# Optimization experiments

Hardware: AMD Instinct MI355X
Metric: run time of the kernel (lower is better)

Reference implementation:

```python
import jax, jax.numpy as jnp
import numpy as np

NUM_CHARTS = 16
LATENT_DIM = 128
RANK = 128
BATCH = 131072


def _init_weight(key, out_dim, in_dim):
    # nn.init.eye_ on top-left block, then += 0.01 * randn (identity-ish init)
    w = jnp.zeros((out_dim, in_dim), jnp.float32)
    m = min(out_dim, in_dim)
    w = w.at[jnp.arange(m), jnp.arange(m)].set(1.0)
    return w + 0.01 * jax.random.normal(key, (out_dim, in_dim), jnp.float32)


def setup_inputs() -> dict:
    key = jax.random.key(0)
    ks = jax.random.split(key, 3 + 2 * NUM_CHARTS)
    z_n = jax.random.normal(ks[0], (BATCH, LATENT_DIM), jnp.float32)
    source_idx = jax.random.randint(ks[1], (BATCH,), 0, NUM_CHARTS, dtype=jnp.int64 if jax.config.jax_enable_x64 else jnp.int32)
    target_idx = jax.random.randint(ks[2], (BATCH,), 0, NUM_CHARTS, dtype=source_idx.dtype)
    # encoder weights: [C, R, D] (torch Linear weight layout [out, in])
    enc_w = jnp.stack([_init_weight(ks[3 + i], RANK, LATENT_DIM) for i in range(NUM_CHARTS)])
    # decoder weights: [C, D, R]
    dec_w = jnp.stack([_init_weight(ks[3 + NUM_CHARTS + i], LATENT_DIM, RANK) for i in range(NUM_CHARTS)])
    c_param = jnp.zeros((NUM_CHARTS, RANK), jnp.float32)
    d_param = jnp.zeros((NUM_CHARTS, LATENT_DIM), jnp.float32)
    return {"z_n": z_n, "source_idx": source_idx, "target_idx": target_idx,
            "enc_w": enc_w, "dec_w": dec_w, "c_param": c_param, "d_param": d_param}


def _apply_per_chart(x, chart_idx, weights):
    # x: [B, in], weights: [C, out, in] -> [B, out]
    # Loop over the small fixed chart count; each chart does one dense GEMM,
    # results routed by mask-select (same math as gather/compute/scatter).
    C = weights.shape[0]
    out = jnp.zeros((x.shape[0], weights.shape[1]), x.dtype)
    for c in range(C):
        yc = x @ weights[c].T  # [B, out]
        out = jnp.where((chart_idx == c)[:, None], yc, out)
    return out


def reference(z_n, source_idx, target_idx, enc_w, dec_w, c_param, d_param):
    # lift_to_global: per-chart encode + bias c[src]
    h = _apply_per_chart(z_n, source_idx, enc_w) + c_param[source_idx]  # [B, R]
    # project_from_global: per-chart decode + bias d[tgt]
    z_out = _apply_per_chart(h, target_idx, dec_w) + d_param[target_idx]  # [B, D]
    return z_out
```

## Files before the change

### kernel.cpp

```cpp
#include <hip/hip_runtime.h>
#include <hip/hip_bf16.h>

#define NB     131072
#define NCH    16
#define NPAIR  256
#define LDW    136
#define LDH    136
#define LDO    132
#define CAP    1024

#define WS_HIST   0
#define WS_OFF    256
#define WS_SORTED 528
#define WS_BYTES  ((WS_SORTED + NB) * 4)

typedef short short8 __attribute__((ext_vector_type(8)));
typedef float f32x4  __attribute__((ext_vector_type(4)));

__device__ __forceinline__ short bfbits(float x) {
    union { __hip_bfloat16 h; short s; } u;
    u.h = __float2bfloat16(x);
    return u.s;
}

__device__ __forceinline__ short8 cvt_frag(const float* __restrict__ p) {
    const f32x4 lo = *(const f32x4*)p;
    const f32x4 hi = *(const f32x4*)(p + 4);
    short8 r;
    r[0] = bfbits(lo[0]); r[1] = bfbits(lo[1]); r[2] = bfbits(lo[2]); r[3] = bfbits(lo[3]);
    r[4] = bfbits(hi[0]); r[5] = bfbits(hi[1]); r[6] = bfbits(hi[2]); r[7] = bfbits(hi[3]);
    return r;
}

__global__ void k_init(int* __restrict__ hist) {
    hist[threadIdx.x] = 0;
}

__global__ __launch_bounds__(256) void k_hist(const int* __restrict__ si,
                                              const int* __restrict__ ti,
                                              int* __restrict__ hist) {
    __shared__ int sh[NPAIR];
    const int t = threadIdx.x;
    sh[t] = 0;
    __syncthreads();
    const int base = blockIdx.x * 1024 + t;
#pragma unroll
    for (int j = 0; j < 4; ++j) {
        const int i = base + j * 256;
        const int k = (si[i] * NCH + ti[i]) & (NPAIR - 1);
        atomicAdd(&sh[k], 1);
    }
    __syncthreads();
    if (sh[t]) atomicAdd(&hist[t], sh[t]);
}

__global__ __launch_bounds__(256) void k_scan(int* __restrict__ hist,
                                              int* __restrict__ off) {
    __shared__ int s[NPAIR];
    const int t = threadIdx.x;
    const int v = hist[t];
    s[t] = v;
    __syncthreads();
#pragma unroll
    for (int d = 1; d < NPAIR; d <<= 1) {
        const int x = (t >= d) ? s[t - d] : 0;
        __syncthreads();
        s[t] += x;
        __syncthreads();
    }
    off[t + 1] = s[t];
    if (t == 0) off[0] = 0;
    hist[t] = s[t] - v;
}

__global__ __launch_bounds__(256) void k_scatter(const int* __restrict__ si,
                                                 const int* __restrict__ ti,
                                                 int* __restrict__ cursor,
                                                 int* __restrict__ sorted) {
    __shared__ int sh[NPAIR];
    __shared__ int sbase[NPAIR];
    const int t = threadIdx.x;
    sh[t] = 0;
    __syncthreads();
    int key[4], rank[4];
    const int base = blockIdx.x * 1024 + t;
#pragma unroll
    for (int j = 0; j < 4; ++j) {
        const int i = base + j * 256;
        const int k = (si[i] * NCH + ti[i]) & (NPAIR - 1);
        key[j]  = k;
        rank[j] = atomicAdd(&sh[k], 1);
    }
    __syncthreads();
    sbase[t] = sh[t] ? atomicAdd(&cursor[t], sh[t]) : 0;
    __syncthreads();
#pragma unroll
    for (int j = 0; j < 4; ++j) {
        const int slot = sbase[key[j]] + rank[j];
        if (slot >= 0 && slot < NB)
            sorted[slot] = base + j * 256;
    }
}

__global__ __launch_bounds__(512, 2)
void k_gemm(const float* __restrict__ z,
            const float* __restrict__ encw,
            const float* __restrict__ decw,
            const float* __restrict__ cpar,
            const float* __restrict__ dpar,
            const int* __restrict__ off,
            const int* __restrict__ sorted,
            float* __restrict__ out) {
    __shared__ int sRowLds[CAP];
    __shared__ __align__(16) __hip_bfloat16 sW1[128 * LDW];
    __shared__ __align__(16) __hip_bfloat16 sW2[128 * LDW];
    __shared__ __align__(16) __hip_bfloat16 sH[8 * 16 * LDH];

    const int bucket = blockIdx.x;
    const int srcc = bucket >> 4;
    const int tgtc = bucket & (NCH - 1);
    const int beg = off[bucket];
    const int end = off[bucket + 1];

    const int tid  = threadIdx.x;
    const int lane = tid & 63;
    const int wv   = tid >> 6;
    const int lr   = lane & 15;
    const int lhi  = lane >> 4;

    {
        const float* W1 = encw + srcc * 16384;
        const float* W2 = decw + tgtc * 16384;
#pragma unroll
        for (int it = 0; it < 4; ++it) {
            const int f = (it * 512 + tid) * 8;
            const int row = f >> 7, col = f & 127;
            *(short8*)(sW1 + row * LDW + col) = cvt_frag(W1 + f);
            *(short8*)(sW2 + row * LDW + col) = cvt_frag(W2 + f);
        }
    }

    float cb[8], db[8];
#pragma unroll
    for (int nt = 0; nt < 8; ++nt) {
        cb[nt] = cpar[srcc * 128 + nt * 16 + lr];
        db[nt] = dpar[tgtc * 128 + nt * 16 + lr];
    }

    __hip_bfloat16* const hs = sH + wv * (16 * LDH);

    auto pf = [&](int g, f32x4* buf) {
        const int rr = sRowLds[(g << 4) + lr];
        const float* p = z + (long)(rr < 0 ? 0 : rr) * 128 + lhi * 8;
#pragma unroll
        for (int k = 0; k < 4; ++k) {
            buf[2 * k]     = *(const f32x4*)(p + k * 32);
            buf[2 * k + 1] = *(const f32x4*)(p + k * 32 + 4);
        }
    };

    auto do_group = [&](int g, const f32x4* buf) {
        f32x4 acc[8];
#pragma unroll
        for (int nt = 0; nt < 8; ++nt) acc[nt] = (f32x4)(0.0f);

#pragma unroll
        for (int k = 0; k < 4; ++k) {
            const f32x4 lo = buf[2 * k], hi = buf[2 * k + 1];
            short8 a;
            a[0] = bfbits(lo[0]); a[1] = bfbits(lo[1]); a[2] = bfbits(lo[2]); a[3] = bfbits(lo[3]);
            a[4] = bfbits(hi[0]); a[5] = bfbits(hi[1]); a[6] = bfbits(hi[2]); a[7] = bfbits(hi[3]);
#pragma unroll
            for (int nt = 0; nt < 8; ++nt) {
                const short8 b = *(const short8*)(sW1 + (nt * 16 + lr) * LDW + k * 32 + lhi * 8);
                acc[nt] = __builtin_amdgcn_mfma_f32_16x16x32_bf16(a, b, acc[nt], 0, 0, 0);
            }
        }

#pragma unroll
        for (int nt = 0; nt < 8; ++nt)
#pragma unroll
            for (int r = 0; r < 4; ++r)
                hs[(lhi * 4 + r) * LDH + nt * 16 + lr] = __float2bfloat16(acc[nt][r] + cb[nt]);

#pragma unroll
        for (int nt = 0; nt < 8; ++nt) acc[nt] = (f32x4)(0.0f);

#pragma unroll
        for (int k = 0; k < 4; ++k) {
            const short8 a = *(const short8*)(hs + lr * LDH + k * 32 + lhi * 8);
#pragma unroll
            for (int nt = 0; nt < 8; ++nt) {
                const short8 b = *(const short8*)(sW2 + (nt * 16 + lr) * LDW + k * 32 + lhi * 8);
                acc[nt] = __builtin_amdgcn_mfma_f32_16x16x32_bf16(a, b, acc[nt], 0, 0, 0);
            }
        }

        int grow[4];
#pragma unroll
        for (int r = 0; r < 4; ++r) grow[r] = sRowLds[(g << 4) + lhi * 4 + r];
#pragma unroll
        for (int nt = 0; nt < 8; ++nt)
#pragma unroll
            for (int r = 0; r < 4; ++r)
                if (grow[r] >= 0)
                    out[(long)grow[r] * 128 + nt * 16 + lr] = acc[nt][r] + db[nt];
    };

    for (int cb0 = beg; cb0 < end; cb0 += CAP) {
        const int cnt = min(end - cb0, CAP);
        __syncthreads();
        for (int i = tid; i < CAP; i += 512) {
            int v = (i < cnt) ? sorted[cb0 + i] : -1;
            sRowLds[i] = ((unsigned)v < (unsigned)NB) ? v : -1;
        }
        __syncthreads();

        const int ng = (cnt + 15) >> 4;
        int g = wv;
        f32x4 pfA[8], pfB[8];
        if (g < ng) pf(g, pfA);
        while (g < ng) {
            int g1 = g + 8;
            if (g1 < ng) pf(g1, pfB);
            do_group(g, pfA);
            g = g1;
            if (g >= ng) break;
            int g2 = g + 8;
            if (g2 < ng) pf(g2, pfA);
            do_group(g, pfB);
            g = g2;
        }
    }
}

__global__ __launch_bounds__(256)
void k_fallback(const float* __restrict__ z,
                const int* __restrict__ si, const int* __restrict__ ti,
                const float* __restrict__ ew,
                const float* __restrict__ dw,
                const float* __restrict__ cp,
                const float* __restrict__ dp,
                float* __restrict__ out) {
    __shared__ float sh[4][128];
    const int lane = threadIdx.x & 63, wv = threadIdx.x >> 6;
    for (int row = blockIdx.x * 4 + wv; row < NB; row += (int)gridDim.x * 4) {
        const int sc = si[row] & (NCH - 1), tc = ti[row] & (NCH - 1);
        const float* zr = z + (long)row * 128;
        const float* W1 = ew + sc * 16384;
        float h0 = cp[sc * 128 + lane];
        float h1 = cp[sc * 128 + lane + 64];
        for (int d = 0; d < 128; ++d) {
            const float zv = zr[d];
            h0 += zv * W1[lane * 128 + d];
            h1 += zv * W1[(lane + 64) * 128 + d];
        }
        sh[wv][lane] = h0;
        sh[wv][lane + 64] = h1;
        __syncthreads();
        const float* W2 = dw + tc * 16384;
        float o0 = dp[tc * 128 + lane];
        float o1 = dp[tc * 128 + lane + 64];
        for (int r = 0; r < 128; ++r) {
            const float hv = sh[wv][r];
            o0 += hv * W2[lane * 128 + r];
            o1 += hv * W2[(lane + 64) * 128 + r];
        }
        out[(long)row * 128 + lane] = o0;
        out[(long)row * 128 + lane + 64] = o1;
        __syncthreads();
    }
}

extern "C" void kernel_launch(void* const* d_in, const int* in_sizes, int n_in,
                              void* d_out, int out_size, void* d_ws, size_t ws_size,
                              hipStream_t stream) {
    const float* z  = (const float*)d_in[0];
    const int*   si = (const int*)d_in[1];
    const int*   ti = (const int*)d_in[2];
    const float* ew = (const float*)d_in[3];
    const float* dw = (const float*)d_in[4];
    const float* cp = (const float*)d_in[5];
    const float* dp = (const float*)d_in[6];
    float* out = (float*)d_out;

    if (ws_size >= (size_t)WS_BYTES) {
        int* hist   = (int*)d_ws + WS_HIST;
        int* off    = (int*)d_ws + WS_OFF;
        int* sorted = (int*)d_ws + WS_SORTED;

        k_init<<<1, NPAIR, 0, stream>>>(hist);
        k_hist<<<128, 256, 0, stream>>>(si, ti, hist);
        k_scan<<<1, NPAIR, 0, stream>>>(hist, off);
        k_scatter<<<128, 256, 0, stream>>>(si, ti, hist, sorted);
        k_gemm<<<NPAIR, 512, 0, stream>>>(z, ew, dw, cp, dp, off, sorted, out);
    } else {
        k_fallback<<<1024, 256, 0, stream>>>(z, si, ti, ew, dw, cp, dp, out);
    }
}
```

Baseline: 146.9 us.

## Process 32-row groups per wave to reuse weight fragments across two MFMA tiles

Each wave now handles 32 rows per group instead of 16, so every B fragment read from shared memory feeds two MFMAs. This halves LDS weight reads per row. The A inputs are converted to bf16 before the next group's prefetch is issued, which replaces the ping-pong buffers with a single-buffer prefetch. In exchange the kernel doubles its accumulator registers, which may hurt occupancy or cause spills under the 512-thread, 2-block launch bounds. It also doubles the per-wave H scratch in LDS and coarsens work granularity for small buckets.

```diff
diff --git a/kernel.cpp b/kernel.cpp
--- a/kernel.cpp
+++ b/kernel.cpp
@@ -26,6 +26,13 @@
 __device__ __forceinline__ short8 cvt_frag(const float* __restrict__ p) {
     const f32x4 lo = *(const f32x4*)p;
     const f32x4 hi = *(const f32x4*)(p + 4);
+    short8 r;
+    r[0] = bfbits(lo[0]); r[1] = bfbits(lo[1]); r[2] = bfbits(lo[2]); r[3] = bfbits(lo[3]);
+    r[4] = bfbits(hi[0]); r[5] = bfbits(hi[1]); r[6] = bfbits(hi[2]); r[7] = bfbits(hi[3]);
+    return r;
+}
+
+__device__ __forceinline__ short8 pack_frag(f32x4 lo, f32x4 hi) {
     short8 r;
     r[0] = bfbits(lo[0]); r[1] = bfbits(lo[1]); r[2] = bfbits(lo[2]); r[3] = bfbits(lo[3]);
     r[4] = bfbits(hi[0]); r[5] = bfbits(hi[1]); r[6] = bfbits(hi[2]); r[7] = bfbits(hi[3]);
@@ -114,7 +121,7 @@
     __shared__ int sRowLds[CAP];
     __shared__ __align__(16) __hip_bfloat16 sW1[128 * LDW];
     __shared__ __align__(16) __hip_bfloat16 sW2[128 * LDW];
-    __shared__ __align__(16) __hip_bfloat16 sH[8 * 16 * LDH];
+    __shared__ __align__(16) __hip_bfloat16 sH[8 * 32 * LDH];
 
     const int bucket = blockIdx.x;
     const int srcc = bucket >> 4;
@@ -147,64 +154,22 @@
         db[nt] = dpar[tgtc * 128 + nt * 16 + lr];
     }
 
-    __hip_bfloat16* const hs = sH + wv * (16 * LDH);
-
-    auto pf = [&](int g, f32x4* buf) {
-        const int rr = sRowLds[(g << 4) + lr];
-        const float* p = z + (long)(rr < 0 ? 0 : rr) * 128 + lhi * 8;
+    __hip_bfloat16* const hs = sH + wv * (32 * LDH);
+
+    f32x4 bufA[8], bufB[8];
+
+    auto pf = [&](int g) {
+        const int r0 = sRowLds[(g << 5) + lr];
+        const int r1 = sRowLds[(g << 5) + 16 + lr];
+        const float* p0 = z + (long)(r0 < 0 ? 0 : r0) * 128 + lhi * 8;
+        const float* p1 = z + (long)(r1 < 0 ? 0 : r1) * 128 + lhi * 8;
 #pragma unroll
         for (int k = 0; k < 4; ++k) {
-            buf[2 * k]     = *(const f32x4*)(p + k * 32);
-            buf[2 * k + 1] = *(const f32x4*)(p + k * 32 + 4);
-        }
-    };
-
-    auto do_group = [&](int g, const f32x4* buf) {
-        f32x4 acc[8];
-#pragma unroll
-        for (int nt = 0; nt < 8; ++nt) acc[nt] = (f32x4)(0.0f);
-
-#pragma unroll
-        for (int k = 0; k < 4; ++k) {
-            const f32x4 lo = buf[2 * k], hi = buf[2 * k + 1];
-            short8 a;
-            a[0] = bfbits(lo[0]); a[1] = bfbits(lo[1]); a[2] = bfbits(lo[2]); a[3] = bfbits(lo[3]);
-            a[4] = bfbits(hi[0]); a[5] = bfbits(hi[1]); a[6] = bfbits(hi[2]); a[7] = bfbits(hi[3]);
-#pragma unroll
-            for (int nt = 0; nt < 8; ++nt) {
-                const short8 b = *(const short8*)(sW1 + (nt * 16 + lr) * LDW + k * 32 + lhi * 8);
-                acc[nt] = __builtin_amdgcn_mfma_f32_16x16x32_bf16(a, b, acc[nt], 0, 0, 0);
-            }
-        }
-
-#pragma unroll
-        for (int nt = 0; nt < 8; ++nt)
-#pragma unroll
-            for (int r = 0; r < 4; ++r)
-                hs[(lhi * 4 + r) * LDH + nt * 16 + lr] = __float2bfloat16(acc[nt][r] + cb[nt]);
-
-#pragma unroll
-        for (int nt = 0; nt < 8; ++nt) acc[nt] = (f32x4)(0.0f);
-
-#pragma unroll
-        for (int k = 0; k < 4; ++k) {
-            const short8 a = *(const short8*)(hs + lr * LDH + k * 32 + lhi * 8);
-#pragma unroll
-            for (int nt = 0; nt < 8; ++nt) {
-                const short8 b = *(const short8*)(sW2 + (nt * 16 + lr) * LDW + k * 32 + lhi * 8);
-                acc[nt] = __builtin_amdgcn_mfma_f32_16x16x32_bf16(a, b, acc[nt], 0, 0, 0);
-            }
-        }
-
-        int grow[4];
-#pragma unroll
-        for (int r = 0; r < 4; ++r) grow[r] = sRowLds[(g << 4) + lhi * 4 + r];
-#pragma unroll
-        for (int nt = 0; nt < 8; ++nt)
-#pragma unroll
-            for (int r = 0; r < 4; ++r)
-                if (grow[r] >= 0)
-                    out[(long)grow[r] * 128 + nt * 16 + lr] = acc[nt][r] + db[nt];
+            bufA[2 * k]     = *(const f32x4*)(p0 + k * 32);
+            bufA[2 * k + 1] = *(const f32x4*)(p0 + k * 32 + 4);
+            bufB[2 * k]     = *(const f32x4*)(p1 + k * 32);
+            bufB[2 * k + 1] = *(const f32x4*)(p1 + k * 32 + 4);
+        }
     };
 
     for (int cb0 = beg; cb0 < end; cb0 += CAP) {
@@ -216,20 +181,74 @@
         }
         __syncthreads();
 
-        const int ng = (cnt + 15) >> 4;
+        const int ng = (cnt + 31) >> 5;
         int g = wv;
-        f32x4 pfA[8], pfB[8];
-        if (g < ng) pf(g, pfA);
+        if (g < ng) pf(g);
         while (g < ng) {
-            int g1 = g + 8;
-            if (g1 < ng) pf(g1, pfB);
-            do_group(g, pfA);
-            g = g1;
-            if (g >= ng) break;
-            int g2 = g + 8;
-            if (g2 < ng) pf(g2, pfA);
-            do_group(g, pfB);
-            g = g2;
+            short8 a0[4], a1[4];
+#pragma unroll
+            for (int k = 0; k < 4; ++k) {
+                a0[k] = pack_frag(bufA[2 * k], bufA[2 * k + 1]);
+                a1[k] = pack_frag(bufB[2 * k], bufB[2 * k + 1]);
+            }
+            const int gn = g + 8;
+            if (gn < ng) pf(gn);
+
+            f32x4 acc0[8], acc1[8];
+#pragma unroll
+            for (int nt = 0; nt < 8; ++nt) { acc0[nt] = (f32x4)(0.0f); acc1[nt] = (f32x4)(0.0f); }
+
+#pragma unroll
+            for (int k = 0; k < 4; ++k) {
+#pragma unroll
+                for (int nt = 0; nt < 8; ++nt) {
+                    const short8 b = *(const short8*)(sW1 + (nt * 16 + lr) * LDW + k * 32 + lhi * 8);
+                    acc0[nt] = __builtin_amdgcn_mfma_f32_16x16x32_bf16(a0[k], b, acc0[nt], 0, 0, 0);
+                    acc1[nt] = __builtin_amdgcn_mfma_f32_16x16x32_bf16(a1[k], b, acc1[nt], 0, 0, 0);
+                }
+            }
+
+#pragma unroll
+            for (int nt = 0; nt < 8; ++nt)
+#pragma unroll
+                for (int r = 0; r < 4; ++r) {
+                    hs[(lhi * 4 + r) * LDH + nt * 16 + lr]        = __float2bfloat16(acc0[nt][r] + cb[nt]);
+                    hs[(16 + lhi * 4 + r) * LDH + nt * 16 + lr]   = __float2bfloat16(acc1[nt][r] + cb[nt]);
+                }
+
+#pragma unroll
+            for (int nt = 0; nt < 8; ++nt) { acc0[nt] = (f32x4)(0.0f); acc1[nt] = (f32x4)(0.0f); }
+
+#pragma unroll
+            for (int k = 0; k < 4; ++k) {
+                const short8 ah0 = *(const short8*)(hs + lr * LDH + k * 32 + lhi * 8);
+                const short8 ah1 = *(const short8*)(hs + (16 + lr) * LDH + k * 32 + lhi * 8);
+#pragma unroll
+                for (int nt = 0; nt < 8; ++nt) {
+                    const short8 b = *(const short8*)(sW2 + (nt * 16 + lr) * LDW + k * 32 + lhi * 8);
+                    acc0[nt] = __builtin_amdgcn_mfma_f32_16x16x32_bf16(ah0, b, acc0[nt], 0, 0, 0);
+                    acc1[nt] = __builtin_amdgcn_mfma_f32_16x16x32_bf16(ah1, b, acc1[nt], 0, 0, 0);
+                }
+            }
+
+            {
+                int g0[4], g1[4];
+#pragma unroll
+                for (int r = 0; r < 4; ++r) {
+                    g0[r] = sRowLds[(g << 5) + lhi * 4 + r];
+                    g1[r] = sRowLds[(g << 5) + 16 + lhi * 4 + r];
+                }
+#pragma unroll
+                for (int nt = 0; nt < 8; ++nt)
+#pragma unroll
+                    for (int r = 0; r < 4; ++r) {
+                        if (g0[r] >= 0)
+                            out[(long)g0[r] * 128 + nt * 16 + lr] = acc0[nt][r] + db[nt];
+                        if (g1[r] >= 0)
+                            out[(long)g1[r] * 128 + nt * 16 + lr] = acc1[nt][r] + db[nt];
+                    }
+            }
+            g = gn;
         }
     }
 }
```

After: 145.4 us. Within noise of the previous version (-1.1%).
